# Kernel optimization log

Hardware: AMD Instinct MI355X
Metric: run time of the kernel (lower is better)

The kernel has to match this reference:

```python
import jax, jax.numpy as jnp
import numpy as np


def setup_inputs() -> dict:
    key = jax.random.key(0)
    kx, ky, kq, kk, kv = jax.random.split(key, 5)
    B, S, D = 4, 4096, 1024
    scale = 1.0 / np.sqrt(D)
    return {
        "X": jax.random.normal(kx, (B, S, D), dtype=jnp.float32),
        "Y": jax.random.normal(ky, (B, S, D), dtype=jnp.float32),
        "Wq": jax.random.normal(kq, (D, D), dtype=jnp.float32) * scale,
        "Wk": jax.random.normal(kk, (D, D), dtype=jnp.float32) * scale,
        "Wv": jax.random.normal(kv, (D, D), dtype=jnp.float32) * scale,
    }


def reference(X, Y, Wq, Wk, Wv):
    # Single-head windowed cross attention.
    # torch nn.Linear(y) == y @ W.T
    WINDOW = 256
    B, S, D = X.shape
    Q = jnp.einsum("bsd,ed->bse", Y, Wq)
    K = jnp.einsum("bsd,ed->bse", X, Wk)
    V = jnp.einsum("bsd,ed->bse", X, Wv)
    scores = jnp.einsum("bqd,bkd->bqk", Q, K) / jnp.sqrt(jnp.float32(D))
    i = jnp.arange(S)
    band = jnp.abs(i[:, None] - i[None, :]) <= WINDOW  # [S, S]
    NEG = jnp.float32(-1e10)  # matches torch masked_fill value
    scores = jnp.where(band[None, :, :], scores, NEG)
    attn = jax.nn.softmax(scores, axis=-1)
    return jnp.einsum("bqk,bkd->bqd", attn, V)
```

## Files before the change

kernel.cpp:

```cpp
#include <hip/hip_runtime.h>
#include <hip/hip_bf16.h>
#include <stdint.h>

typedef _Float16 half8 __attribute__((ext_vector_type(8)));
typedef float floatx4 __attribute__((ext_vector_type(4)));

#define MFMA16(a, b, c) __builtin_amdgcn_mfma_f32_16x16x32_f16(a, b, c, 0, 0, 0)

__device__ __forceinline__ void async_load16(const void* g, void* l) {
    __builtin_amdgcn_global_load_lds((__attribute__((address_space(1))) void*)(g),
                                     (__attribute__((address_space(3))) void*)(l),
                                     16, 0, 0);
}


__global__ __launch_bounds__(256) void cvt_kernel(const float* __restrict__ in,
                                                  _Float16* __restrict__ out,
                                                  int n, float scale) {
    int i = (blockIdx.x * 256 + threadIdx.x) * 8;
    if (i >= n) return;
    float4 v0 = *(const float4*)(in + i);
    float4 v1 = *(const float4*)(in + i + 4);
    half8 h;
    h[0] = (_Float16)(v0.x * scale);
    h[1] = (_Float16)(v0.y * scale);
    h[2] = (_Float16)(v0.z * scale);
    h[3] = (_Float16)(v0.w * scale);
    h[4] = (_Float16)(v1.x * scale);
    h[5] = (_Float16)(v1.y * scale);
    h[6] = (_Float16)(v1.z * scale);
    h[7] = (_Float16)(v1.w * scale);
    *(half8*)(out + i) = h;
}

__global__ __launch_bounds__(512, 2) void gemm_bt(const _Float16* __restrict__ A,
                                                  const _Float16* __restrict__ B,
                                                  _Float16* __restrict__ C,
                                                  int M, int N, int K) {
    __shared__ _Float16 sA[2][256 * 32];
    __shared__ _Float16 sB[2][256 * 32];
    const int tid  = threadIdx.x;
    const int lane = tid & 63;
    const int w    = tid >> 6;
    const int quad = lane >> 4;
    const int m16  = lane & 15;
    const int wm   = (w >> 2) * 128;
    const int wn   = (w & 3) * 64;

    const int gx = gridDim.x, gy = gridDim.y;
    const int total = gx * gy;
    const int id = blockIdx.y * gx + blockIdx.x;
    const int logical = (id & 7) * (total >> 3) + (id >> 3);
    int bx, by;
    if (gx <= gy) { bx = logical % gx; by = logical / gx; }
    else          { by = logical % gy; bx = logical / gy; }
    const long row0 = (long)by * 256;
    const long col0 = (long)bx * 256;

    floatx4 acc[8][4] = {};

    const int swz = ((tid & 3) ^ ((tid >> 3) & 3)) * 8;
    const _Float16* ga0 = A + (row0 + (tid >> 2)) * (long)K + swz;
    const _Float16* ga1 = ga0 + 128l * K;
    const _Float16* gb0 = B + (col0 + (tid >> 2)) * (long)K + swz;
    const _Float16* gb1 = gb0 + 128l * K;
    const int wchunk = w * 1024;

    auto stage = [&](int bi, int kc) {
        char* lA = (char*)sA[bi] + wchunk;
        char* lB = (char*)sB[bi] + wchunk;
        async_load16(ga0 + kc, lA);
        async_load16(ga1 + kc, lA + 8192);
        async_load16(gb0 + kc, lB);
        async_load16(gb1 + kc, lB + 8192);
    };

    const int rswz = (m16 >> 1) & 3;

    stage(0, 0);
    for (int kc = 0; kc < K; kc += 32) {
        const int bi = (kc >> 5) & 1;
        __syncthreads();
        if (kc + 32 < K) stage(bi ^ 1, kc + 32);
        half8 af[8], bf[4];
#pragma unroll
        for (int mt = 0; mt < 8; mt++)
            af[mt] = *(const half8*)(sA[bi] + (wm + mt * 16 + m16) * 32 + (quad ^ rswz) * 8);
#pragma unroll
        for (int nt = 0; nt < 4; nt++)
            bf[nt] = *(const half8*)(sB[bi] + (wn + nt * 16 + m16) * 32 + (quad ^ rswz) * 8);
#pragma unroll
        for (int mt = 0; mt < 8; mt++)
#pragma unroll
            for (int nt = 0; nt < 4; nt++)
                acc[mt][nt] = MFMA16(af[mt], bf[nt], acc[mt][nt]);
    }

#pragma unroll
    for (int mt = 0; mt < 8; mt++)
#pragma unroll
        for (int nt = 0; nt < 4; nt++)
#pragma unroll
            for (int reg = 0; reg < 4; reg++) {
                long r = row0 + wm + mt * 16 + quad * 4 + reg;
                long c = col0 + wn + nt * 16 + m16;
                C[r * N + c] = (_Float16)acc[mt][nt][reg];
            }
}

__global__ __launch_bounds__(512) void qk_kernel(const _Float16* __restrict__ Qh,
                                                 const _Float16* __restrict__ Kh,
                                                 _Float16* __restrict__ Pg,
                                                 float* __restrict__ invSum) {
    const int S = 4096, D = 1024;
    __shared__ _Float16 sK[2][576 * 32];
    __shared__ _Float16 sQ[2][64 * 32];
    __shared__ float sMax[64][8];
    __shared__ float sSum[64][8];

    const int tid  = threadIdx.x;
    const int lane = tid & 63;
    const int w    = tid >> 6;
    const int quad = lane >> 4;
    const int c16  = lane & 15;
    const int qblk = (blockIdx.x & 7) * 32 + (blockIdx.x >> 3);
    const int b    = qblk >> 6;
    const int q0   = (qblk & 63) << 6;

    int kstart = q0 - 256; if (kstart < 0) kstart = 0;
    int kend   = q0 + 320; if (kend > S) kend = S;
    const int L = kend - kstart;
    const int ntiles = L >> 4;

    const int lrow = lane >> 2;
    const int swz  = ((lane & 3) ^ ((lane >> 3) & 3)) * 8;
    const _Float16* Kbase = Kh + ((long)(b * S + kstart) + lrow) * D + swz;
    const _Float16* Qbase = Qh + ((long)(b * S + q0) + w * 16 + lrow) * D + swz;

    auto stage = [&](int bi, int kc) {
#pragma unroll
        for (int j = 0; j < 5; j++) {
            int g = j * 8 + w;
            if (g < ntiles)
                async_load16(Kbase + (long)g * 16 * D + kc, (char*)sK[bi] + g * 1024);
        }
        if (w < 4)
            async_load16(Qbase + kc, (char*)sQ[bi] + w * 1024);
    };

    const int rswz = ((c16 >> 1) & 3);

    floatx4 acc[4][5] = {};
    stage(0, 0);
    for (int kc = 0; kc < 1024; kc += 32) {
        const int bi = (kc >> 5) & 1;
        __syncthreads();
        if (kc + 32 < 1024) stage(bi ^ 1, kc + 32);
        half8 aQ[4];
#pragma unroll
        for (int mt = 0; mt < 4; mt++)
            aQ[mt] = *(const half8*)(sQ[bi] + (mt * 16 + c16) * 32 + (quad ^ rswz) * 8);
#pragma unroll
        for (int i = 0; i < 5; i++) {
            int t = w + i * 8;
            if (t < ntiles) {
                half8 bK = *(const half8*)(sK[bi] + (t * 16 + c16) * 32 + (quad ^ rswz) * 8);
#pragma unroll
                for (int mt = 0; mt < 4; mt++)
                    acc[mt][i] = MFMA16(aQ[mt], bK, acc[mt][i]);
            }
        }
    }

#pragma unroll
    for (int i = 0; i < 5; i++) {
        int t = w + i * 8;
        if (t < ntiles) {
            int j = kstart + t * 16 + c16;
#pragma unroll
            for (int mt = 0; mt < 4; mt++)
#pragma unroll
                for (int r = 0; r < 4; r++) {
                    int qi = q0 + mt * 16 + quad * 4 + r;
                    int dd = qi - j; dd = dd < 0 ? -dd : dd;
                    if (dd > 256) acc[mt][i][r] = -1e30f;
                }
        }
    }
#pragma unroll
    for (int mt = 0; mt < 4; mt++)
#pragma unroll
        for (int r = 0; r < 4; r++) {
            float m = -1e30f;
#pragma unroll
            for (int i = 0; i < 5; i++)
                if (w + i * 8 < ntiles) m = fmaxf(m, acc[mt][i][r]);
#pragma unroll
            for (int off = 1; off < 16; off <<= 1) m = fmaxf(m, __shfl_xor(m, off, 64));
            if (c16 == 0) sMax[mt * 16 + quad * 4 + r][w] = m;
        }
    __syncthreads();
    if (tid < 64) {
        float fm = sMax[tid][0];
#pragma unroll
        for (int j = 1; j < 8; j++) fm = fmaxf(fm, sMax[tid][j]);
        sMax[tid][0] = fm;
    }
    __syncthreads();
#pragma unroll
    for (int mt = 0; mt < 4; mt++)
#pragma unroll
        for (int r = 0; r < 4; r++) {
            int row = mt * 16 + quad * 4 + r;
            float fm = sMax[row][0];
            float s = 0.f;
#pragma unroll
            for (int i = 0; i < 5; i++) {
                int t = w + i * 8;
                if (t < ntiles) {
                    float e = __expf(acc[mt][i][r] - fm);
                    s += e;
                    Pg[(long)qblk * 36864 + row * 576 + t * 16 + c16] = (_Float16)e;
                }
            }
#pragma unroll
            for (int off = 1; off < 16; off <<= 1) s += __shfl_xor(s, off, 64);
            if (c16 == 0) sSum[row][w] = s;
        }
    __syncthreads();
    if (tid < 64) {
        float t = 0.f;
#pragma unroll
        for (int j = 0; j < 8; j++) t += sSum[tid][j];
        invSum[qblk * 64 + tid] = 1.f / t;
    }
}

__global__ __launch_bounds__(512) void pv_kernel(const _Float16* __restrict__ Pg,
                                                 const float* __restrict__ invSum,
                                                 const _Float16* __restrict__ Vt,
                                                 float* __restrict__ out) {
    const int S = 4096, D = 1024, TOK = 16384;
    __shared__ _Float16 sA[2][64 * 32];
    __shared__ _Float16 sB[2][256 * 32];

    const int tid  = threadIdx.x;
    const int lane = tid & 63;
    const int w    = tid >> 6;
    const int quad = lane >> 4;
    const int c16  = lane & 15;

    const int logical = (blockIdx.x & 7) * 128 + (blockIdx.x >> 3);
    const int qblk = logical >> 2;
    const int n0   = (logical & 3) << 8;
    const int b    = qblk >> 6;
    const int q0   = (qblk & 63) << 6;

    int kstart = q0 - 256; if (kstart < 0) kstart = 0;
    int kend   = q0 + 320; if (kend > S) kend = S;
    const int nsteps = (kend - kstart) >> 5;

    const int lrow = lane >> 2;
    const int swz  = ((lane & 3) ^ ((lane >> 3) & 3)) * 8;
    const _Float16* Abase = Pg + (long)qblk * 36864 + (w * 16 + lrow) * 576 + swz;
    const _Float16* Bbase = Vt + (long)(n0 + lrow) * TOK + b * S + kstart + swz;

    auto stage = [&](int bi, int kc) {
        if (w < 4)
            async_load16(Abase + kc, (char*)sA[bi] + w * 1024);
#pragma unroll
        for (int j = 0; j < 2; j++) {
            int g = j * 8 + w;
            async_load16(Bbase + (long)g * 16 * TOK + kc, (char*)sB[bi] + g * 1024);
        }
    };

    const int wm = (w >> 2) * 32;
    const int wn = (w & 3) * 64;
    const int rswz = ((c16 >> 1) & 3);
    floatx4 acc[2][4] = {};

    stage(0, 0);
    for (int s = 0; s < nsteps; s++) {
        const int bi = s & 1;
        __syncthreads();
        if (s + 1 < nsteps) stage(bi ^ 1, (s + 1) * 32);
        half8 aA[2], bB[4];
#pragma unroll
        for (int mt = 0; mt < 2; mt++)
            aA[mt] = *(const half8*)(sA[bi] + (wm + mt * 16 + c16) * 32 + (quad ^ rswz) * 8);
#pragma unroll
        for (int nt = 0; nt < 4; nt++)
            bB[nt] = *(const half8*)(sB[bi] + (wn + nt * 16 + c16) * 32 + (quad ^ rswz) * 8);
#pragma unroll
        for (int mt = 0; mt < 2; mt++)
#pragma unroll
            for (int nt = 0; nt < 4; nt++)
                acc[mt][nt] = MFMA16(aA[mt], bB[nt], acc[mt][nt]);
    }

    const float* isB = invSum + qblk * 64;
#pragma unroll
    for (int mt = 0; mt < 2; mt++)
#pragma unroll
        for (int nt = 0; nt < 4; nt++)
#pragma unroll
            for (int reg = 0; reg < 4; reg++) {
                int row = wm + mt * 16 + quad * 4 + reg;
                int col = n0 + wn + nt * 16 + c16;
                out[(long)(b * S + q0 + row) * D + col] = acc[mt][nt][reg] * isB[row];
            }
}

extern "C" void kernel_launch(void* const* d_in, const int* in_sizes, int n_in,
                              void* d_out, int out_size, void* d_ws, size_t ws_size,
                              hipStream_t stream) {
    const float* X  = (const float*)d_in[0];
    const float* Y  = (const float*)d_in[1];
    const float* Wq = (const float*)d_in[2];
    const float* Wk = (const float*)d_in[3];
    const float* Wv = (const float*)d_in[4];
    float* out = (float*)d_out;

    const long NTOK = 16384, D = 1024;
    char* p = (char*)d_ws;
    _Float16* Xh  = (_Float16*)p; p += NTOK * D * 2;
    _Float16* Yh  = (_Float16*)p; p += NTOK * D * 2;
    _Float16* Wqh = (_Float16*)p; p += D * D * 2;
    _Float16* Wkh = (_Float16*)p; p += D * D * 2;
    _Float16* Wvh = (_Float16*)p; p += D * D * 2;
    _Float16* Qh  = (_Float16*)p; p += NTOK * D * 2;
    _Float16* Vt  = (_Float16*)p; p += NTOK * D * 2;
    _Float16* Kh  = Yh;
    _Float16* Pg  = Xh;
    float* invSum = (float*)(Xh + 256l * 64 * 576);

    const int nT = (int)(NTOK * D);
    const int nW = (int)(D * D);
    cvt_kernel<<<nT / 2048, 256, 0, stream>>>(X, Xh, nT, 1.f);
    cvt_kernel<<<nT / 2048, 256, 0, stream>>>(Y, Yh, nT, 1.f);
    cvt_kernel<<<nW / 2048, 256, 0, stream>>>(Wq, Wqh, nW, 0.03125f);
    cvt_kernel<<<nW / 2048, 256, 0, stream>>>(Wk, Wkh, nW, 1.f);
    cvt_kernel<<<nW / 2048, 256, 0, stream>>>(Wv, Wvh, nW, 1.f);

    gemm_bt<<<dim3(1024 / 256, 16384 / 256), 512, 0, stream>>>(Yh, Wqh, Qh, 16384, 1024, 1024);
    gemm_bt<<<dim3(1024 / 256, 16384 / 256), 512, 0, stream>>>(Xh, Wkh, Kh, 16384, 1024, 1024);
    gemm_bt<<<dim3(16384 / 256, 1024 / 256), 512, 0, stream>>>(Wvh, Xh, Vt, 1024, 16384, 1024);

    qk_kernel<<<dim3(256), 512, 0, stream>>>(Qh, Kh, Pg, invSum);
    pv_kernel<<<dim3(4 * 256), 512, 0, stream>>>(Pg, invSum, Vt, out);
}
```

Before: 410.3 us.

## Restructure projection GEMM into four-phase pipelined K=64 loop with raw barriers

The projection GEMM now works on K=64 tiles held as two 32-wide LDS slabs. Each tile's compute is split into four quadrant phases, and the async global->LDS loads for the next two tiles are interleaved across those phases. Explicit s_barrier, vmcnt/lgkmcnt waits and setprio replace __syncthreads, so memory traffic overlaps with MFMA work and the compiler's conservative waits are avoided. The change doubles LDS use to 128KB per block, which can lower occupancy from the declared 2 blocks per CU, and manual waitcnt counts risk hazards if they are miscounted.

Result: faster. 377.3 us (-8.0%).

```diff
diff --git a/kernel.cpp b/kernel.cpp
--- a/kernel.cpp
+++ b/kernel.cpp
@@ -12,6 +12,10 @@
                                      (__attribute__((address_space(3))) void*)(l),
                                      16, 0, 0);
 }
+
+#define RAW_BARRIER()  asm volatile("s_barrier" ::: "memory")
+#define WAIT_VMCNT(n)  asm volatile("s_waitcnt vmcnt(" #n ")" ::: "memory")
+#define WAIT_LGKM0()   asm volatile("s_waitcnt lgkmcnt(0)" ::: "memory")
 
 
 __global__ __launch_bounds__(256) void cvt_kernel(const float* __restrict__ in,
@@ -37,15 +41,15 @@
                                                   const _Float16* __restrict__ B,
                                                   _Float16* __restrict__ C,
                                                   int M, int N, int K) {
-    __shared__ _Float16 sA[2][256 * 32];
-    __shared__ _Float16 sB[2][256 * 32];
+    __shared__ _Float16 sA[2][2][256 * 32];
+    __shared__ _Float16 sB[2][2][256 * 32];
     const int tid  = threadIdx.x;
     const int lane = tid & 63;
     const int w    = tid >> 6;
     const int quad = lane >> 4;
     const int m16  = lane & 15;
-    const int wm   = (w >> 2) * 128;
-    const int wn   = (w & 3) * 64;
+    const int mq   = (w >> 2) * 64;
+    const int nq   = (w & 3) * 32;
 
     const int gx = gridDim.x, gy = gridDim.y;
     const int total = gx * gy;
@@ -60,50 +64,90 @@
     floatx4 acc[8][4] = {};
 
     const int swz = ((tid & 3) ^ ((tid >> 3) & 3)) * 8;
-    const _Float16* ga0 = A + (row0 + (tid >> 2)) * (long)K + swz;
-    const _Float16* ga1 = ga0 + 128l * K;
-    const _Float16* gb0 = B + (col0 + (tid >> 2)) * (long)K + swz;
-    const _Float16* gb1 = gb0 + 128l * K;
+    const _Float16* ga = A + (row0 + (tid >> 2)) * (long)K + swz;
+    const _Float16* gb = B + (col0 + (tid >> 2)) * (long)K + swz;
     const int wchunk = w * 1024;
 
-    auto stage = [&](int bi, int kc) {
-        char* lA = (char*)sA[bi] + wchunk;
-        char* lB = (char*)sB[bi] + wchunk;
-        async_load16(ga0 + kc, lA);
-        async_load16(ga1 + kc, lA + 8192);
-        async_load16(gb0 + kc, lB);
-        async_load16(gb1 + kc, lB + 8192);
+    auto stageA = [&](int tile, int half) {
+        const int s = tile & 1;
+        char* l0 = (char*)sA[s][0] + half * 8192 + wchunk;
+        char* l1 = (char*)sA[s][1] + half * 8192 + wchunk;
+        const _Float16* g = ga + (long)tile * 64 + (long)half * 128 * K;
+        async_load16(g, l0);
+        async_load16(g + 32, l1);
     };
+    auto stageB = [&](int tile, int half) {
+        const int s = tile & 1;
+        char* l0 = (char*)sB[s][0] + half * 8192 + wchunk;
+        char* l1 = (char*)sB[s][1] + half * 8192 + wchunk;
+        const _Float16* g = gb + (long)tile * 64 + (long)half * 128 * K;
+        async_load16(g, l0);
+        async_load16(g + 32, l1);
+    };
 
     const int rswz = (m16 >> 1) & 3;
-
-    stage(0, 0);
-    for (int kc = 0; kc < K; kc += 32) {
-        const int bi = (kc >> 5) & 1;
-        __syncthreads();
-        if (kc + 32 < K) stage(bi ^ 1, kc + 32);
-        half8 af[8], bf[4];
-#pragma unroll
-        for (int mt = 0; mt < 8; mt++)
-            af[mt] = *(const half8*)(sA[bi] + (wm + mt * 16 + m16) * 32 + (quad ^ rswz) * 8);
+    const int NTt  = K >> 6;
+
+    stageA(0, 0); stageA(0, 1); stageB(0, 0); stageB(0, 1);
+    stageA(1, 0); stageB(1, 0);
+    WAIT_VMCNT(4);
+    RAW_BARRIER();
+
+    for (int U = 0; U < NTt; ++U) {
+        const int s = U & 1;
+        const int T1 = U + 1, T2 = U + 2;
+        half8 af[4][2], bf[2][2];
+#pragma unroll
+        for (int p = 0; p < 4; ++p) {
+            const int mh = p >> 1, nh = p & 1;
+            if ((p & 1) == 0) {
+#pragma unroll
+                for (int mt = 0; mt < 4; mt++)
+#pragma unroll
+                    for (int j = 0; j < 2; j++)
+                        af[mt][j] = *(const half8*)(sA[s][j] +
+                            (mh * 128 + mq + mt * 16 + m16) * 32 + (quad ^ rswz) * 8);
+            }
+#pragma unroll
+            for (int nt = 0; nt < 2; nt++)
+#pragma unroll
+                for (int j = 0; j < 2; j++)
+                    bf[nt][j] = *(const half8*)(sB[s][j] +
+                        (nh * 128 + nq + nt * 16 + m16) * 32 + (quad ^ rswz) * 8);
+            if (p == 0 && T1 < NTt) stageB(T1, 1);
+            if (p == 1 && T1 < NTt) stageA(T1, 1);
+            if (p == 2 && T2 < NTt) stageA(T2, 0);
+            if (p == 3 && T2 < NTt) stageB(T2, 0);
+            if (p == 3) {
+                if (T2 < NTt) { WAIT_VMCNT(4); }
+                else          { WAIT_VMCNT(0); }
+            }
+            RAW_BARRIER();
+            WAIT_LGKM0();
+            __builtin_amdgcn_sched_barrier(0);
+            __builtin_amdgcn_s_setprio(1);
+#pragma unroll
+            for (int mt = 0; mt < 4; mt++)
+#pragma unroll
+                for (int nt = 0; nt < 2; nt++) {
+                    acc[mh * 4 + mt][nh * 2 + nt] =
+                        MFMA16(af[mt][0], bf[nt][0], acc[mh * 4 + mt][nh * 2 + nt]);
+                    acc[mh * 4 + mt][nh * 2 + nt] =
+                        MFMA16(af[mt][1], bf[nt][1], acc[mh * 4 + mt][nh * 2 + nt]);
+                }
+            __builtin_amdgcn_s_setprio(0);
+            RAW_BARRIER();
+        }
+    }
+
+#pragma unroll
+    for (int mt = 0; mt < 8; mt++)
 #pragma unroll
         for (int nt = 0; nt < 4; nt++)
-            bf[nt] = *(const half8*)(sB[bi] + (wn + nt * 16 + m16) * 32 + (quad ^ rswz) * 8);
-#pragma unroll
-        for (int mt = 0; mt < 8; mt++)
-#pragma unroll
-            for (int nt = 0; nt < 4; nt++)
-                acc[mt][nt] = MFMA16(af[mt], bf[nt], acc[mt][nt]);
-    }
-
-#pragma unroll
-    for (int mt = 0; mt < 8; mt++)
-#pragma unroll
-        for (int nt = 0; nt < 4; nt++)
 #pragma unroll
             for (int reg = 0; reg < 4; reg++) {
-                long r = row0 + wm + mt * 16 + quad * 4 + reg;
-                long c = col0 + wn + nt * 16 + m16;
+                long r = row0 + (mt >> 2) * 128 + mq + (mt & 3) * 16 + quad * 4 + reg;
+                long c = col0 + (nt >> 1) * 128 + nq + (nt & 1) * 16 + m16;
                 C[r * N + c] = (_Float16)acc[mt][nt][reg];
             }
 }
```
